# Kernel optimization log

Hardware: AMD Instinct MI355X
Metric: run time of the kernel (lower is better)

Reference implementation:

```python
import jax, jax.numpy as jnp
import numpy as np
from jax import lax

B, C, HID, G = 32, 16, 128, 256
FIRE_RATE = 0.5


def _make_filters(n_channels):
    # identity, sobel_x, sobel_y (sobel scaled by 1/8), tiled per channel:
    # torch stacks [id, sx, sy] then .repeat((C,1,1)) -> pattern repeats every 3
    sobel = jnp.array([[-1., 0., 1.], [-2., 0., 2.], [-1., 0., 1.]], dtype=jnp.float32)
    sx = sobel / 8.0
    sy = sobel.T / 8.0
    ident = jnp.zeros((3, 3), dtype=jnp.float32).at[1, 1].set(1.0)
    f = jnp.stack([ident, sx, sy])                        # [3,3,3]
    f = jnp.tile(f, (n_channels, 1, 1))                   # [3C,3,3]
    return f[:, None, :, :]                               # [3C,1,3,3] OIHW


def _living_mask(x):
    # max_pool2d(k=3, s=1, pad=1) on alpha channel (index 3), threshold 0.1
    alpha = x[:, 3:4, :, :]
    pooled = lax.reduce_window(alpha, -jnp.inf, lax.max,
                               (1, 1, 3, 3), (1, 1, 1, 1), 'SAME')
    return pooled > 0.1  # [B,1,H,W] bool


def setup_inputs() -> dict:
    key = jax.random.key(0)
    k0, k1, k2, k3 = jax.random.split(key, 4)
    x = jax.random.normal(k0, (B, C, G, G), dtype=jnp.float32)
    w1 = jax.random.normal(k1, (HID, 3 * C), dtype=jnp.float32) * 0.1  # conv1 1x1 weight
    b1 = jnp.zeros((HID,), dtype=jnp.float32)
    # original zero-inits w2; use small random values so the op is non-trivial
    w2 = jax.random.normal(k2, (C, HID), dtype=jnp.float32) * 0.02     # conv2 1x1 weight (no bias)
    update_mask = (jax.random.uniform(k3, (B, 1, G, G)) <= FIRE_RATE).astype(jnp.float32)
    return {"x": x, "w1": w1, "b1": b1, "w2": w2, "update_mask": update_mask}


def reference(x, w1, b1, w2, update_mask):
    n_channels = x.shape[1]
    filt = _make_filters(n_channels)
    pre_life = _living_mask(x)
    # perceive: depthwise (groups=C) 3x3 conv, 3 filters per channel
    y = lax.conv_general_dilated(
        x, filt, window_strides=(1, 1), padding='SAME',
        dimension_numbers=('NCHW', 'OIHW', 'NCHW'),
        feature_group_count=n_channels)                    # [B,3C,H,W]
    # update: 1x1 conv -> ReLU -> 1x1 conv (per-pixel MLP)
    h = jax.nn.relu(jnp.einsum('bchw,kc->bkhw', y, w1) + b1[None, :, None, None])
    dx = jnp.einsum('bkhw,ck->bchw', h, w2)
    # stochastic update (no scaling)
    dx = dx * update_mask
    x_new = x + dx
    post_life = _living_mask(x_new)
    life = (pre_life & post_life).astype(x.dtype)
    return x_new * life
```

## Files before the change

### kernel.cpp

```cpp
#include <hip/hip_runtime.h>

#define G    256
#define CCH  16
#define HIDN 128
#define TS   16
#define LDSW 19

__global__ __launch_bounds__(256) void nca_compute(
    const float* __restrict__ x, const float* __restrict__ w1,
    const float* __restrict__ b1, const float* __restrict__ w2,
    const float* __restrict__ um, float* __restrict__ out,
    float* __restrict__ alpha_new)
{
    __shared__ float xs[CCH][18 * LDSW];
    const int tx = threadIdx.x, ty = threadIdx.y;
    const int bx = blockIdx.x * TS, by = blockIdx.y * TS, b = blockIdx.z;
    const int tid = ty * TS + tx;

    const float* xb = x + (size_t)b * CCH * G * G;
    for (int i = tid; i < CCH * 18 * 18; i += 256) {
        int c   = i / (18 * 18);
        int rem = i % (18 * 18);
        int r   = rem / 18;
        int col = rem % 18;
        int gy = by + r - 1, gx = bx + col - 1;
        float v = 0.f;
        if (gy >= 0 && gy < G && gx >= 0 && gx < G)
            v = xb[(size_t)c * G * G + (size_t)gy * G + gx];
        xs[c][r * LDSW + col] = v;
    }
    __syncthreads();

    float y[48];
    #pragma unroll
    for (int c = 0; c < CCH; c++) {
        float a00 = xs[c][(ty    ) * LDSW + tx    ];
        float a01 = xs[c][(ty    ) * LDSW + tx + 1];
        float a02 = xs[c][(ty    ) * LDSW + tx + 2];
        float a10 = xs[c][(ty + 1) * LDSW + tx    ];
        float a11 = xs[c][(ty + 1) * LDSW + tx + 1];
        float a12 = xs[c][(ty + 1) * LDSW + tx + 2];
        float a20 = xs[c][(ty + 2) * LDSW + tx    ];
        float a21 = xs[c][(ty + 2) * LDSW + tx + 1];
        float a22 = xs[c][(ty + 2) * LDSW + tx + 2];
        y[3 * c]     = a11;
        y[3 * c + 1] = ((a02 - a00) + 2.f * (a12 - a10) + (a22 - a20)) * 0.125f;
        y[3 * c + 2] = ((a20 - a00) + 2.f * (a21 - a01) + (a22 - a02)) * 0.125f;
    }

    float acc[CCH];
    #pragma unroll
    for (int c = 0; c < CCH; c++) acc[c] = 0.f;

    for (int k = 0; k < HIDN; k++) {
        const float* w1r = w1 + k * 48;
        float h0 = b1[k], h1 = 0.f, h2 = 0.f, h3 = 0.f;
        #pragma unroll
        for (int c = 0; c < 48; c += 4) {
            h0 = fmaf(w1r[c    ], y[c    ], h0);
            h1 = fmaf(w1r[c + 1], y[c + 1], h1);
            h2 = fmaf(w1r[c + 2], y[c + 2], h2);
            h3 = fmaf(w1r[c + 3], y[c + 3], h3);
        }
        float hk = fmaxf((h0 + h1) + (h2 + h3), 0.f);
        #pragma unroll
        for (int c = 0; c < CCH; c++)
            acc[c] = fmaf(w2[c * HIDN + k], hk, acc[c]);
    }

    const int gy = by + ty, gx = bx + tx;
    const float m = um[(size_t)b * G * G + (size_t)gy * G + gx];
    const size_t pix   = (size_t)gy * G + gx;
    const size_t obase = (size_t)b * CCH * G * G + pix;
    #pragma unroll
    for (int c = 0; c < CCH; c++) {
        float xn = xs[c][(ty + 1) * LDSW + tx + 1] + acc[c] * m;
        out[obase + (size_t)c * G * G] = xn;
        if (c == 3) alpha_new[(size_t)b * G * G + pix] = xn;
    }
}

__global__ __launch_bounds__(256) void nca_mask(
    const float* __restrict__ x, const float* __restrict__ alpha_new,
    float* __restrict__ out)
{
    __shared__ float pa[18 * LDSW];
    __shared__ float na[18 * LDSW];
    const int tx = threadIdx.x, ty = threadIdx.y;
    const int bx = blockIdx.x * TS, by = blockIdx.y * TS, b = blockIdx.z;
    const int tid = ty * TS + tx;

    const float* xa = x + (size_t)b * CCH * G * G + (size_t)3 * G * G;
    const float* nb = alpha_new + (size_t)b * G * G;
    for (int i = tid; i < 18 * 18; i += 256) {
        int r = i / 18, col = i % 18;
        int gy = by + r - 1, gx = bx + col - 1;
        float vp = -1e30f, vn = -1e30f;
        if (gy >= 0 && gy < G && gx >= 0 && gx < G) {
            vp = xa[(size_t)gy * G + gx];
            vn = nb[(size_t)gy * G + gx];
        }
        pa[r * LDSW + col] = vp;
        na[r * LDSW + col] = vn;
    }
    __syncthreads();

    float mp = -1e30f, mn = -1e30f;
    #pragma unroll
    for (int dy = 0; dy < 3; dy++) {
        #pragma unroll
        for (int dx = 0; dx < 3; dx++) {
            mp = fmaxf(mp, pa[(ty + dy) * LDSW + tx + dx]);
            mn = fmaxf(mn, na[(ty + dy) * LDSW + tx + dx]);
        }
    }
    const bool life = (mp > 0.1f) && (mn > 0.1f);
    if (!life) {
        const size_t obase = (size_t)b * CCH * G * G + (size_t)(by + ty) * G + (bx + tx);
        #pragma unroll
        for (int c = 0; c < CCH; c++)
            out[obase + (size_t)c * G * G] = 0.f;
    }
}

extern "C" void kernel_launch(void* const* d_in, const int* in_sizes, int n_in,
                              void* d_out, int out_size, void* d_ws, size_t ws_size,
                              hipStream_t stream) {
    const float* x  = (const float*)d_in[0];
    const float* w1 = (const float*)d_in[1];
    const float* b1 = (const float*)d_in[2];
    const float* w2 = (const float*)d_in[3];
    const float* um = (const float*)d_in[4];
    float* out = (float*)d_out;
    float* alpha_new = (float*)d_ws;

    dim3 grid(G / TS, G / TS, 32);
    dim3 block(TS, TS);
    nca_compute<<<grid, block, 0, stream>>>(x, w1, b1, w2, um, out, alpha_new);
    nca_mask<<<grid, block, 0, stream>>>(x, alpha_new, out);
}
```

Baseline: 816.2 us.

## Stage MLP weights in LDS and fold pre-life mask into compute kernel

Loads w1, a transposed w2 and b1 into shared memory, reusing the input tile buffer after the perceive step, and reads them as float4 vectors instead of per-thread global loads. The pre-update living mask is now computed in the compute kernel from the alpha tile already in LDS, so the mask kernel only reads the new alpha. Adds a launch-bounds occupancy hint and an extra block barrier, and the LDS footprint grows to hold the weights.

Result: slower. 1.285 ms (+57.5%).

```diff
diff --git a/kernel.cpp b/kernel.cpp
--- a/kernel.cpp
+++ b/kernel.cpp
@@ -6,13 +6,19 @@
 #define TS   16
 #define LDSW 19
 
-__global__ __launch_bounds__(256) void nca_compute(
+#define XS_FLOATS  (CCH * 18 * LDSW)
+#define W1_FLOATS  (HIDN * 48)
+#define W2T_FLOATS (HIDN * CCH)
+#define WTOT       (W1_FLOATS + W2T_FLOATS + HIDN)
+#define LDS_FLOATS (WTOT > XS_FLOATS ? WTOT : XS_FLOATS)
+
+__global__ __launch_bounds__(256, 4) void nca_compute(
     const float* __restrict__ x, const float* __restrict__ w1,
     const float* __restrict__ b1, const float* __restrict__ w2,
     const float* __restrict__ um, float* __restrict__ out,
     float* __restrict__ alpha_new)
 {
-    __shared__ float xs[CCH][18 * LDSW];
+    __shared__ __align__(16) float lds[LDS_FLOATS];
     const int tx = threadIdx.x, ty = threadIdx.y;
     const int bx = blockIdx.x * TS, by = blockIdx.y * TS, b = blockIdx.z;
     const int tid = ty * TS + tx;
@@ -27,95 +33,124 @@
         float v = 0.f;
         if (gy >= 0 && gy < G && gx >= 0 && gx < G)
             v = xb[(size_t)c * G * G + (size_t)gy * G + gx];
-        xs[c][r * LDSW + col] = v;
+        lds[c * (18 * LDSW) + r * LDSW + col] = v;
     }
     __syncthreads();
 
     float y[48];
     #pragma unroll
     for (int c = 0; c < CCH; c++) {
-        float a00 = xs[c][(ty    ) * LDSW + tx    ];
-        float a01 = xs[c][(ty    ) * LDSW + tx + 1];
-        float a02 = xs[c][(ty    ) * LDSW + tx + 2];
-        float a10 = xs[c][(ty + 1) * LDSW + tx    ];
-        float a11 = xs[c][(ty + 1) * LDSW + tx + 1];
-        float a12 = xs[c][(ty + 1) * LDSW + tx + 2];
-        float a20 = xs[c][(ty + 2) * LDSW + tx    ];
-        float a21 = xs[c][(ty + 2) * LDSW + tx + 1];
-        float a22 = xs[c][(ty + 2) * LDSW + tx + 2];
+        const float* xc = lds + c * (18 * LDSW);
+        float a00 = xc[(ty    ) * LDSW + tx    ];
+        float a01 = xc[(ty    ) * LDSW + tx + 1];
+        float a02 = xc[(ty    ) * LDSW + tx + 2];
+        float a10 = xc[(ty + 1) * LDSW + tx    ];
+        float a11 = xc[(ty + 1) * LDSW + tx + 1];
+        float a12 = xc[(ty + 1) * LDSW + tx + 2];
+        float a20 = xc[(ty + 2) * LDSW + tx    ];
+        float a21 = xc[(ty + 2) * LDSW + tx + 1];
+        float a22 = xc[(ty + 2) * LDSW + tx + 2];
         y[3 * c]     = a11;
         y[3 * c + 1] = ((a02 - a00) + 2.f * (a12 - a10) + (a22 - a20)) * 0.125f;
         y[3 * c + 2] = ((a20 - a00) + 2.f * (a21 - a01) + (a22 - a02)) * 0.125f;
     }
+
+    float mp = -1e30f;
+    {
+        const float* xa = lds + 3 * (18 * LDSW);
+        #pragma unroll
+        for (int dy = 0; dy < 3; dy++)
+            #pragma unroll
+            for (int dx = 0; dx < 3; dx++)
+                mp = fmaxf(mp, xa[(ty + dy) * LDSW + tx + dx]);
+    }
+    const bool pre = mp > 0.1f;
+    const int gy = by + ty, gx = bx + tx;
+    const float m = um[(size_t)b * G * G + (size_t)gy * G + gx];
+
+    __syncthreads();
+
+    {
+        const float4* w1v = (const float4*)w1;
+        float4* dst = (float4*)lds;
+        for (int i = tid; i < W1_FLOATS / 4; i += 256) dst[i] = w1v[i];
+        float* ws2t = lds + W1_FLOATS;
+        for (int i = tid; i < W2T_FLOATS; i += 256) {
+            int c = i >> 7, k = i & 127;
+            ws2t[k * CCH + c] = w2[i];
+        }
+        float* wb1 = lds + W1_FLOATS + W2T_FLOATS;
+        for (int i = tid; i < HIDN; i += 256) wb1[i] = b1[i];
+    }
+    __syncthreads();
+
+    const float* ws2t = lds + W1_FLOATS;
+    const float* wb1  = lds + W1_FLOATS + W2T_FLOATS;
 
     float acc[CCH];
     #pragma unroll
     for (int c = 0; c < CCH; c++) acc[c] = 0.f;
 
     for (int k = 0; k < HIDN; k++) {
-        const float* w1r = w1 + k * 48;
-        float h0 = b1[k], h1 = 0.f, h2 = 0.f, h3 = 0.f;
+        const float4* w1r = (const float4*)(lds + k * 48);
+        float h0 = wb1[k], h1 = 0.f, h2 = 0.f, h3 = 0.f;
         #pragma unroll
-        for (int c = 0; c < 48; c += 4) {
-            h0 = fmaf(w1r[c    ], y[c    ], h0);
-            h1 = fmaf(w1r[c + 1], y[c + 1], h1);
-            h2 = fmaf(w1r[c + 2], y[c + 2], h2);
-            h3 = fmaf(w1r[c + 3], y[c + 3], h3);
+        for (int q = 0; q < 12; q++) {
+            float4 w = w1r[q];
+            h0 = fmaf(w.x, y[4 * q    ], h0);
+            h1 = fmaf(w.y, y[4 * q + 1], h1);
+            h2 = fmaf(w.z, y[4 * q + 2], h2);
+            h3 = fmaf(w.w, y[4 * q + 3], h3);
         }
         float hk = fmaxf((h0 + h1) + (h2 + h3), 0.f);
+        const float4* w2r = (const float4*)(ws2t + k * CCH);
         #pragma unroll
-        for (int c = 0; c < CCH; c++)
-            acc[c] = fmaf(w2[c * HIDN + k], hk, acc[c]);
+        for (int q = 0; q < 4; q++) {
+            float4 w = w2r[q];
+            acc[4 * q    ] = fmaf(w.x, hk, acc[4 * q    ]);
+            acc[4 * q + 1] = fmaf(w.y, hk, acc[4 * q + 1]);
+            acc[4 * q + 2] = fmaf(w.z, hk, acc[4 * q + 2]);
+            acc[4 * q + 3] = fmaf(w.w, hk, acc[4 * q + 3]);
+        }
     }
 
-    const int gy = by + ty, gx = bx + tx;
-    const float m = um[(size_t)b * G * G + (size_t)gy * G + gx];
     const size_t pix   = (size_t)gy * G + gx;
     const size_t obase = (size_t)b * CCH * G * G + pix;
     #pragma unroll
     for (int c = 0; c < CCH; c++) {
-        float xn = xs[c][(ty + 1) * LDSW + tx + 1] + acc[c] * m;
-        out[obase + (size_t)c * G * G] = xn;
+        float xn = y[3 * c] + acc[c] * m;
         if (c == 3) alpha_new[(size_t)b * G * G + pix] = xn;
+        out[obase + (size_t)c * G * G] = pre ? xn : 0.f;
     }
 }
 
 __global__ __launch_bounds__(256) void nca_mask(
-    const float* __restrict__ x, const float* __restrict__ alpha_new,
-    float* __restrict__ out)
+    const float* __restrict__ alpha_new, float* __restrict__ out)
 {
-    __shared__ float pa[18 * LDSW];
     __shared__ float na[18 * LDSW];
     const int tx = threadIdx.x, ty = threadIdx.y;
     const int bx = blockIdx.x * TS, by = blockIdx.y * TS, b = blockIdx.z;
     const int tid = ty * TS + tx;
 
-    const float* xa = x + (size_t)b * CCH * G * G + (size_t)3 * G * G;
     const float* nb = alpha_new + (size_t)b * G * G;
     for (int i = tid; i < 18 * 18; i += 256) {
         int r = i / 18, col = i % 18;
         int gy = by + r - 1, gx = bx + col - 1;
-        float vp = -1e30f, vn = -1e30f;
-        if (gy >= 0 && gy < G && gx >= 0 && gx < G) {
-            vp = xa[(size_t)gy * G + gx];
+        float vn = -1e30f;
+        if (gy >= 0 && gy < G && gx >= 0 && gx < G)
             vn = nb[(size_t)gy * G + gx];
-        }
-        pa[r * LDSW + col] = vp;
         na[r * LDSW + col] = vn;
     }
     __syncthreads();
 
-    float mp = -1e30f, mn = -1e30f;
+    float mn = -1e30f;
     #pragma unroll
-    for (int dy = 0; dy < 3; dy++) {
+    for (int dy = 0; dy < 3; dy++)
         #pragma unroll
-        for (int dx = 0; dx < 3; dx++) {
-            mp = fmaxf(mp, pa[(ty + dy) * LDSW + tx + dx]);
+        for (int dx = 0; dx < 3; dx++)
             mn = fmaxf(mn, na[(ty + dy) * LDSW + tx + dx]);
-        }
-    }
-    const bool life = (mp > 0.1f) && (mn > 0.1f);
-    if (!life) {
+
+    if (!(mn > 0.1f)) {
         const size_t obase = (size_t)b * CCH * G * G + (size_t)(by + ty) * G + (bx + tx);
         #pragma unroll
         for (int c = 0; c < CCH; c++)
@@ -137,5 +172,5 @@
     dim3 grid(G / TS, G / TS, 32);
     dim3 block(TS, TS);
     nca_compute<<<grid, block, 0, stream>>>(x, w1, b1, w2, um, out, alpha_new);
-    nca_mask<<<grid, block, 0, stream>>>(x, alpha_new, out);
+    nca_mask<<<grid, block, 0, stream>>>(alpha_new, out);
 }
```
